# Kernel optimization log

Hardware: AMD Instinct MI355X
Metric: run time of the kernel (lower is better)

Reference implementation:

```python
import jax, jax.numpy as jnp
import numpy as np

NUM_GROUPS = 16   # static upper bound on group ids (actual ids in [0, 12))
MIN_COUNT = 10    # min_subgroup_count


def setup_inputs() -> dict:
    key = jax.random.key(0)
    ks = jax.random.split(key, 7)
    B = 32768
    N = 16777216  # dataset_size
    probs = jax.random.uniform(ks[0], (B,), dtype=jnp.float32)
    labels = jax.random.randint(ks[1], (B,), 0, 2, dtype=jnp.int32)
    groups = jax.random.randint(ks[2], (B,), 0, 12, dtype=jnp.int32)
    indices = jax.random.randint(ks[3], (B,), 0, N, dtype=jnp.int32)
    # persistent buffers, pre-filled with valid mid-epoch state
    score_buffer = jax.random.uniform(ks[4], (N,), dtype=jnp.float32)
    label_buffer = jax.random.randint(ks[5], (N,), 0, 2, dtype=jnp.int32)
    group_buffer = jax.random.randint(ks[6], (N,), 0, 12, dtype=jnp.int32)
    return {"probs": probs, "labels": labels, "groups": groups, "indices": indices,
            "score_buffer": score_buffer, "label_buffer": label_buffer,
            "group_buffer": group_buffer}


def reference(probs, labels, groups, indices, score_buffer, label_buffer, group_buffer):
    # scatter current batch into dataset-sized buffers (functional clone + write)
    scores = score_buffer.at[indices].set(probs)
    labs = label_buffer.at[indices].set(labels)
    grps = group_buffer.at[indices].set(groups)

    valid = (~jnp.isnan(scores)) & (labs >= 0) & (grps >= 0)
    scores = jnp.where(valid, scores, 0.0)        # kill NaNs before weighted sums
    seg = jnp.where(valid, grps, 0)               # invalid rows get weight 0 anyway

    def group_var(lab_val):
        # per-group mean of scores restricted to (valid & label==lab_val),
        # then unbiased variance across groups meeting the min-count threshold
        w = (valid & (labs == lab_val)).astype(scores.dtype)
        sums = jax.ops.segment_sum(scores * w, seg, num_segments=NUM_GROUPS)
        cnts = jax.ops.segment_sum(w, seg, num_segments=NUM_GROUPS)
        avg = sums / jnp.maximum(cnts, 1.0)
        incl = (cnts >= MIN_COUNT).astype(scores.dtype)
        n = incl.sum()
        mean = (avg * incl).sum() / jnp.maximum(n, 1.0)
        var = (incl * (avg - mean) ** 2).sum() / jnp.maximum(n - 1.0, 1.0)  # ddof=1
        return var, n

    pos_var, n_pos = group_var(1)
    neg_var, n_neg = group_var(0)
    pos_ok = n_pos >= 2.0
    neg_ok = n_neg >= 2.0
    loss = jnp.where(pos_ok & neg_ok, 0.5 * (pos_var + neg_var),
                     jnp.where(pos_ok, pos_var,
                               jnp.where(neg_ok, neg_var, 0.0)))
    return loss
```

## Files before the change

### kernel.cpp

```cpp
#include <hip/hip_runtime.h>
#include <hip/hip_bf16.h>


#define TBL   65536u
#define TBLM  (TBL - 1u)
#define NGR   12
#define NBK   24
#define NCOL  25
#define CCOL  26
#define NTHR  256
#define CHUNK 16384
#define ITER  (CHUNK / 4 / NTHR)
#define UNR   4
#define MINC  10.0

__device__ __forceinline__ unsigned hash_idx(unsigned idx) {
    return (idx * 2654435761u) & TBLM;
}

__global__ void k_vote(const int* __restrict__ indices,
                       unsigned long long* __restrict__ table,
                       unsigned* __restrict__ bitmap, int B) {
    int b = blockIdx.x * blockDim.x + threadIdx.x;
    if (b >= B) return;
    unsigned idx = (unsigned)indices[b];
    atomicOr(&bitmap[idx >> 5], 1u << (idx & 31u));
    unsigned long long key = ((unsigned long long)(idx + 1u)) << 32;
    unsigned long long val = key | (unsigned long long)(unsigned)b;
    unsigned slot = hash_idx(idx);
    for (;;) {
        unsigned long long prev = atomicCAS(&table[slot], 0ULL, val);
        if (prev == 0ULL) return;
        if ((prev >> 32) == (unsigned long long)(idx + 1u)) {
            atomicMax(&table[slot], val);
            return;
        }
        slot = (slot + 1u) & TBLM;
    }
}

__global__ void k_resolve(const unsigned long long* __restrict__ table,
                          const float* __restrict__ probs,
                          const int* __restrict__ labels,
                          const int* __restrict__ groups,
                          float4* __restrict__ tbl2) {
    int s = blockIdx.x * blockDim.x + threadIdx.x;
    unsigned long long e = table[s];
    unsigned hi = (unsigned)(e >> 32);
    float4 r = make_float4(0.f, 0.f, 0.f, 0.f);
    if (hi) {
        int b = (int)(e & 0xffffffffu);
        r.x = probs[b];
        r.y = __int_as_float(labels[b]);
        r.z = __int_as_float(groups[b]);
        r.w = __uint_as_float(hi);
    }
    tbl2[s] = r;
}

__device__ __forceinline__ void apply_ovr(int idx, float& s, int& l, int& g,
        const float4* __restrict__ tbl2) {
    unsigned slot = hash_idx((unsigned)idx);
    unsigned hi = (unsigned)idx + 1u;
    for (;;) {
        float4 r = tbl2[slot];
        if (__float_as_uint(r.w) == hi) {
            s = r.x; l = __float_as_int(r.y); g = __float_as_int(r.z);
            return;
        }
        slot = (slot + 1u) & TBLM;
    }
}

__device__ __forceinline__ float ovr_s(int idx,
        const float4* __restrict__ tbl2) {
    unsigned slot = hash_idx((unsigned)idx);
    unsigned hi = (unsigned)idx + 1u;
    for (;;) {
        float4 r = tbl2[slot];
        if (__float_as_uint(r.w) == hi) return r.x;
        slot = (slot + 1u) & TBLM;
    }
}

__device__ __forceinline__ void quad_p1(float* __restrict__ row,
        unsigned* __restrict__ bstr32,
        float4 s4, int4 l4, int4 g4, unsigned bits, int v,
        const float4* __restrict__ tbl2) {
    float ss[4] = {s4.x, s4.y, s4.z, s4.w};
    int   ll[4] = {l4.x, l4.y, l4.z, l4.w};
    int   gg[4] = {g4.x, g4.y, g4.z, g4.w};
    if (bits & 0xFu) {
#pragma unroll
        for (int e = 0; e < 4; ++e)
            if ((bits >> e) & 1u)
                apply_ovr((v << 2) + e, ss[e], ll[e], gg[e], tbl2);
    }
    float val[4]; int bkt[4];
#pragma unroll
    for (int e = 0; e < 4; ++e) {
        bool valid = (ss[e] == ss[e]) && ((unsigned)ll[e] < 2u) &&
                     ((unsigned)gg[e] < (unsigned)NGR);
        bkt[e] = valid ? (gg[e] * 2 + ll[e]) : NBK;
        val[e] = valid ? ss[e] : 0.f;
    }
    bstr32[v] = (unsigned)bkt[0] | ((unsigned)bkt[1] << 8) |
                ((unsigned)bkt[2] << 16) | ((unsigned)bkt[3] << 24);
#define MRG(i, j) { bool m_ = (bkt[i] == bkt[j]); \
                    val[i] += m_ ? val[j] : 0.f;  \
                    bkt[j] = m_ ? NBK : bkt[j];   \
                    val[j] = m_ ? 0.f : val[j]; }
    MRG(0,1) MRG(0,2) MRG(0,3) MRG(1,2) MRG(1,3) MRG(2,3)
#undef MRG
    float a0 = row[bkt[0]], a1 = row[bkt[1]], a2 = row[bkt[2]], a3 = row[bkt[3]];
    row[bkt[0]] = a0 + val[0];
    row[bkt[1]] = a1 + val[1];
    row[bkt[2]] = a2 + val[2];
    row[bkt[3]] = a3 + val[3];
}

__global__ __launch_bounds__(NTHR, 4) void k_pass1(
        const float* __restrict__ sb, const int* __restrict__ lb,
        const int* __restrict__ gb, const unsigned* __restrict__ bitmap,
        const float4* __restrict__ tbl2,
        float* __restrict__ bsum, unsigned char* __restrict__ bstream,
        int n, int nblk) {
    __shared__ float s_acc[NTHR * NCOL];
    int tid = threadIdx.x, blk = blockIdx.x;
    for (int i = tid; i < NTHR * NCOL; i += NTHR) s_acc[i] = 0.f;
    __syncthreads();
    float* row = &s_acc[tid * NCOL];
    unsigned* bstr32 = (unsigned*)bstream;
    int vbase = (blk * CHUNK) >> 2, nv = n >> 2;
    if (vbase + (CHUNK >> 2) <= nv) {
        int v0 = vbase + tid;
        unsigned sh = (unsigned)((v0 & 7) * 4);
#pragma unroll
        for (int m = 0; m < ITER / UNR; ++m) {
            float4 s4[UNR]; int4 l4[UNR], g4[UNR]; unsigned bm[UNR];
#pragma unroll
            for (int u = 0; u < UNR; ++u) {
                int v = v0 + (m * UNR + u) * NTHR;
                s4[u] = ((const float4*)sb)[v];
                l4[u] = ((const int4*)lb)[v];
                g4[u] = ((const int4*)gb)[v];
                bm[u] = bitmap[v >> 3];
            }
            asm volatile("" ::: "memory");
#pragma unroll
            for (int u = 0; u < UNR; ++u) {
                int v = v0 + (m * UNR + u) * NTHR;
                quad_p1(row, bstr32, s4[u], l4[u], g4[u], bm[u] >> sh, v, tbl2);
            }
        }
    } else {
        for (int it = 0; it < ITER; ++it) {
            int v = vbase + it * NTHR + tid;
            if (v >= nv) break;
            float4 s4 = ((const float4*)sb)[v];
            int4   l4 = ((const int4*)lb)[v];
            int4   g4 = ((const int4*)gb)[v];
            unsigned bits = bitmap[v >> 3] >> ((v & 7) * 4);
            quad_p1(row, bstr32, s4, l4, g4, bits, v, tbl2);
        }
    }
    if (blk == nblk - 1) {
        for (int i = (nv << 2) + tid; i < n; i += NTHR) {
            float s = sb[i]; int l = lb[i], g = gb[i];
            if ((bitmap[i >> 5] >> (i & 31)) & 1u)
                apply_ovr(i, s, l, g, tbl2);
            bool valid = (s == s) && ((unsigned)l < 2u) && ((unsigned)g < (unsigned)NGR);
            int bk = valid ? (g * 2 + l) : NBK;
            bstream[i] = (unsigned char)bk;
            row[bk] += valid ? s : 0.f;
        }
    }
    __syncthreads();
    if (tid < NBK * 8) {
        int bkt = tid >> 3, sub = tid & 7;
        float sm = 0.f;
        for (int j = 0; j < 32; ++j) sm += s_acc[(sub * 32 + j) * NCOL + bkt];
        for (int d = 4; d >= 1; d >>= 1) sm += __shfl_down(sm, d, 8);
        if (!sub) bsum[bkt * nblk + blk] = sm;
    }
}

__global__ void k_scan(const float* __restrict__ bsum,
                       float* __restrict__ bpref, int nblk) {
    __shared__ double sc[NTHR];
    int t = threadIdx.x, k = blockIdx.x;
    const float* src = bsum  + (size_t)k * nblk;
    float*       dst = bpref + (size_t)k * nblk;
    double carry = 0.0;
    for (int s0 = 0; s0 < nblk; s0 += 4 * NTHR) {
        int i0 = s0 + 4 * t;
        float x0 = (i0 + 0 < nblk) ? src[i0 + 0] : 0.f;
        float x1 = (i0 + 1 < nblk) ? src[i0 + 1] : 0.f;
        float x2 = (i0 + 2 < nblk) ? src[i0 + 2] : 0.f;
        float x3 = (i0 + 3 < nblk) ? src[i0 + 3] : 0.f;
        double p0 = (double)x0, p1 = p0 + x1, p2 = p1 + x2, tot = p2 + x3;
        sc[t] = tot;
        __syncthreads();
        for (int st = 1; st < NTHR; st <<= 1) {
            double a = (t >= st) ? sc[t - st] : 0.0;
            __syncthreads();
            sc[t] += a;
            __syncthreads();
        }
        double excl = carry + sc[t] - tot;
        if (i0 + 0 < nblk) dst[i0 + 0] = (float)excl;
        if (i0 + 1 < nblk) dst[i0 + 1] = (float)(excl + p0);
        if (i0 + 2 < nblk) dst[i0 + 2] = (float)(excl + p1);
        if (i0 + 3 < nblk) dst[i0 + 3] = (float)(excl + p2);
        double bt = sc[NTHR - 1];
        __syncthreads();
        carry += bt;
    }
}

__device__ __forceinline__ double aload_d(const double* p) {
    unsigned long long u = __hip_atomic_load((const unsigned long long*)p,
                              __ATOMIC_RELAXED, __HIP_MEMORY_SCOPE_AGENT);
    return __longlong_as_double((long long)u);
}

__device__ __forceinline__ void quad_p2(float* __restrict__ row,
        unsigned short* __restrict__ crow,
        const float2* __restrict__ s_model,
        float4 s4, unsigned b4, unsigned obits, int v, int base,
        const float4* __restrict__ tbl2) {
    float ss[4] = {s4.x, s4.y, s4.z, s4.w};
    if (obits & 0xFu) {
#pragma unroll
        for (int e = 0; e < 4; ++e)
            if ((obits >> e) & 1u) ss[e] = ovr_s((v << 2) + e, tbl2);
    }
    float cv[4]; int bkt[4], cn[4];
#pragma unroll
    for (int e = 0; e < 4; ++e) {
        int idx = (v << 2) + e;
        int bk = (int)((b4 >> (8 * e)) & 0xFFu);
        float s = ss[e];
        float2 m = s_model[bk];
        float S = fmaf(m.y, (float)(idx - base), m.x);
        float T = S + s;
        unsigned ue = __float_as_uint(T) & 0x7f800000u;
        float c;
        if (ue < (24u << 23)) c = s;
        else {
            unsigned ub = ue - (23u << 23);
            float u    = __uint_as_float(ub);
            float uinv = __uint_as_float((254u << 23) - ub);
            c = u * rintf(s * uinv);
        }
        bool valid = bk < NBK;
        bkt[e] = bk;
        cv[e] = valid ? c : 0.f;
        cn[e] = valid ? 1 : 0;
    }
#define MRG(i, j) { bool m_ = (bkt[i] == bkt[j]); \
                    cv[i] += m_ ? cv[j] : 0.f;    \
                    cn[i] += m_ ? cn[j] : 0;      \
                    bkt[j] = m_ ? NBK : bkt[j];   \
                    cv[j] = m_ ? 0.f : cv[j];     \
                    cn[j] = m_ ? 0 : cn[j]; }
    MRG(0,1) MRG(0,2) MRG(0,3) MRG(1,2) MRG(1,3) MRG(2,3)
#undef MRG
    float a0 = row[bkt[0]], a1 = row[bkt[1]], a2 = row[bkt[2]], a3 = row[bkt[3]];
    row[bkt[0]] = a0 + cv[0];
    row[bkt[1]] = a1 + cv[1];
    row[bkt[2]] = a2 + cv[2];
    row[bkt[3]] = a3 + cv[3];
    unsigned short c0 = crow[bkt[0]], c1 = crow[bkt[1]],
                   c2 = crow[bkt[2]], c3 = crow[bkt[3]];
    crow[bkt[0]] = (unsigned short)(c0 + cn[0]);
    crow[bkt[1]] = (unsigned short)(c1 + cn[1]);
    crow[bkt[2]] = (unsigned short)(c2 + cn[2]);
    crow[bkt[3]] = (unsigned short)(c3 + cn[3]);
}

__global__ __launch_bounds__(NTHR, 4) void k_pass2(
        const float* __restrict__ sb,
        const unsigned char* __restrict__ bstream,
        const unsigned* __restrict__ bitmap,
        const float4* __restrict__ tbl2,
        const float* __restrict__ bsum, const float* __restrict__ bpref,
        double* __restrict__ acc_sum, double* __restrict__ acc_cnt,
        unsigned* __restrict__ done, float* __restrict__ out,
        int n, int nblk) {
    __shared__ float s_accv[NTHR * NCOL];
    __shared__ unsigned short s_cnt[NTHR * CCOL];
    __shared__ float2 s_model[NCOL];
    int tid = threadIdx.x, blk = blockIdx.x;
    for (int i = tid; i < NTHR * NCOL; i += NTHR) s_accv[i] = 0.f;
    for (int i = tid; i < NTHR * CCOL; i += NTHR) s_cnt[i] = 0;
    if (tid < NBK)
        s_model[tid] = make_float2(bpref[tid * nblk + blk],
                                   bsum[tid * nblk + blk] * (1.0f / CHUNK));
    if (tid == NBK) s_model[NBK] = make_float2(0.f, 0.f);
    __syncthreads();
    float* row = &s_accv[tid * NCOL];
    unsigned short* crow = &s_cnt[tid * CCOL];
    const unsigned* bstr32 = (const unsigned*)bstream;
    int base = blk * CHUNK;
    int vbase = base >> 2, nv = n >> 2;
    if (vbase + (CHUNK >> 2) <= nv) {
        int v0 = vbase + tid;
        unsigned sh = (unsigned)((v0 & 7) * 4);
#pragma unroll
        for (int m = 0; m < ITER / UNR; ++m) {
            float4 s4[UNR]; unsigned pk[UNR], bm[UNR];
#pragma unroll
            for (int u = 0; u < UNR; ++u) {
                int v = v0 + (m * UNR + u) * NTHR;
                s4[u] = ((const float4*)sb)[v];
                pk[u] = bstr32[v];
                bm[u] = bitmap[v >> 3];
            }
            asm volatile("" ::: "memory");
#pragma unroll
            for (int u = 0; u < UNR; ++u) {
                int v = v0 + (m * UNR + u) * NTHR;
                quad_p2(row, crow, s_model, s4[u], pk[u], bm[u] >> sh,
                        v, base, tbl2);
            }
        }
    } else {
        for (int it = 0; it < ITER; ++it) {
            int v = vbase + it * NTHR + tid;
            if (v >= nv) break;
            float4 s4 = ((const float4*)sb)[v];
            unsigned b4 = bstr32[v];
            unsigned bits = bitmap[v >> 3] >> ((v & 7) * 4);
            quad_p2(row, crow, s_model, s4, b4, bits, v, base, tbl2);
        }
    }
    if (blk == nblk - 1) {
        for (int i = (nv << 2) + tid; i < n; i += NTHR) {
            float s = sb[i];
            int bk = (int)bstream[i];
            if ((bitmap[i >> 5] >> (i & 31)) & 1u)
                s = ovr_s(i, tbl2);
            float2 m = s_model[bk];
            float S = fmaf(m.y, (float)(i - base), m.x);
            float T = S + s;
            unsigned ue = __float_as_uint(T) & 0x7f800000u;
            float c;
            if (ue < (24u << 23)) c = s;
            else {
                unsigned ub = ue - (23u << 23);
                float u    = __uint_as_float(ub);
                float uinv = __uint_as_float((254u << 23) - ub);
                c = u * rintf(s * uinv);
            }
            bool valid = bk < NBK;
            row[bk] += valid ? c : 0.f;
            crow[bk] = (unsigned short)(crow[bk] + (valid ? 1 : 0));
        }
    }
    __syncthreads();
    if (tid < NBK * 8) {
        int bkt = tid >> 3, sub = tid & 7;
        float sm = 0.f; unsigned cc = 0;
        for (int j = 0; j < 32; ++j) {
            int t2 = sub * 32 + j;
            sm += s_accv[t2 * NCOL + bkt];
            cc += s_cnt[t2 * CCOL + bkt];
        }
        for (int d = 4; d >= 1; d >>= 1) {
            sm += __shfl_down(sm, d, 8);
            cc += __shfl_down(cc, d, 8);
        }
        if (!sub) {
            atomicAdd(&acc_sum[bkt], (double)sm);
            atomicAdd(&acc_cnt[bkt], (double)cc);
        }
    }
    __syncthreads();
    if (tid == 0) {
        __threadfence();
        unsigned r = __hip_atomic_fetch_add(done, 1u, __ATOMIC_ACQ_REL,
                                            __HIP_MEMORY_SCOPE_AGENT);
        if (r == (unsigned)(gridDim.x - 1)) {
            double var[2], nn[2];
            for (int l = 0; l < 2; ++l) {
                double avg[NGR];
                double ncnt = 0.0, s = 0.0;
                for (int g = 0; g < NGR; ++g) {
                    double c  = aload_d(&acc_cnt[g * 2 + l]);
                    double sm = aload_d(&acc_sum[g * 2 + l]);
                    double a = sm / fmax(c, 1.0);
                    avg[g] = a;
                    if (c >= MINC) { ncnt += 1.0; s += a; }
                }
                double mean = s / fmax(ncnt, 1.0), v = 0.0;
                for (int g = 0; g < NGR; ++g) {
                    double c = aload_d(&acc_cnt[g * 2 + l]);
                    if (c >= MINC) { double d = avg[g] - mean; v += d * d; }
                }
                var[l] = v / fmax(ncnt - 1.0, 1.0);
                nn[l] = ncnt;
            }
            bool p = nn[1] >= 2.0, q = nn[0] >= 2.0;
            double loss = (p && q) ? 0.5 * (var[1] + var[0])
                        : (p ? var[1] : (q ? var[0] : 0.0));
            out[0] = (float)loss;
        }
    }
}

extern "C" void kernel_launch(void* const* d_in, const int* in_sizes, int n_in,
                              void* d_out, int out_size, void* d_ws, size_t ws_size,
                              hipStream_t stream) {
    const float* probs   = (const float*)d_in[0];
    const int*   labels  = (const int*)d_in[1];
    const int*   groups  = (const int*)d_in[2];
    const int*   indices = (const int*)d_in[3];
    const float* sb      = (const float*)d_in[4];
    const int*   lb      = (const int*)d_in[5];
    const int*   gb      = (const int*)d_in[6];
    int B = in_sizes[0];
    int n = in_sizes[4];
    int nblk   = (n + CHUNK - 1) / CHUNK;
    int nwords = (n + 31) / 32;

    char* ws = (char*)d_ws;
    size_t off = 0;
    unsigned long long* table = (unsigned long long*)(ws + off); off += (size_t)TBL * 8;
    unsigned* bitmap  = (unsigned*)(ws + off); off += (size_t)nwords * 4;
    off = (off + 15) & ~(size_t)15;
    double*   acc_sum = (double*)(ws + off);   off += NBK * 8;
    double*   acc_cnt = (double*)(ws + off);   off += NBK * 8;
    unsigned* done    = (unsigned*)(ws + off); off += 16;
    size_t zero_bytes = off;
    float4*   tbl2    = (float4*)(ws + off);   off += (size_t)TBL * 16;
    unsigned char* bstream = (unsigned char*)(ws + off);
    off += ((size_t)n + 15) & ~(size_t)15;
    float*    bsum    = (float*)(ws + off);    off += (size_t)nblk * NBK * 4;
    float*    bpref   = (float*)(ws + off);    off += (size_t)nblk * NBK * 4;

    hipMemsetAsync(d_ws, 0, zero_bytes, stream);

    dim3 bblk((B + NTHR - 1) / NTHR);
    hipLaunchKernelGGL(k_vote, bblk, dim3(NTHR), 0, stream,
                       indices, table, bitmap, B);
    hipLaunchKernelGGL(k_resolve, dim3(TBL / NTHR), dim3(NTHR), 0, stream,
                       table, probs, labels, groups, tbl2);
    hipLaunchKernelGGL(k_pass1, dim3(nblk), dim3(NTHR), 0, stream,
                       sb, lb, gb, bitmap, tbl2, bsum, bstream, n, nblk);
    hipLaunchKernelGGL(k_scan, dim3(NBK), dim3(NTHR), 0, stream,
                       bsum, bpref, nblk);
    hipLaunchKernelGGL(k_pass2, dim3(nblk), dim3(NTHR), 0, stream,
                       sb, bstream, bitmap, tbl2, bsum, bpref,
                       acc_sum, acc_cnt, done, (float*)d_out, n, nblk);
}
```

Baseline: 305.1 us.

## Move overridden-row handling out of the streaming loops into a sparse bitmap sweep

Overridden rows are now marked invalid (bucket NBK) in the pass-1 stream, and both passes process them afterwards in a separate per-block sweep. That sweep walks bitmap words with ctz and does the hash lookups there. This removes per-quad bitmap loads and divergent hash probing from the hot loops of pass 2, and lets pass 2 unroll deeper (8 instead of 4). The cost is an extra bitmap scan per block. The quantisation term for overridden rows is still computed against the block prefix model, but its in-chunk order differs from the original, which could change rounding slightly.

```diff
diff --git a/kernel.cpp b/kernel.cpp
--- a/kernel.cpp
+++ b/kernel.cpp
@@ -11,7 +11,8 @@
 #define NTHR  256
 #define CHUNK 16384
 #define ITER  (CHUNK / 4 / NTHR)
-#define UNR   4
+#define UNR1  4
+#define UNR2  8
 #define MINC  10.0
 
 __device__ __forceinline__ unsigned hash_idx(unsigned idx) {
@@ -72,34 +73,17 @@
     }
 }
 
-__device__ __forceinline__ float ovr_s(int idx,
-        const float4* __restrict__ tbl2) {
-    unsigned slot = hash_idx((unsigned)idx);
-    unsigned hi = (unsigned)idx + 1u;
-    for (;;) {
-        float4 r = tbl2[slot];
-        if (__float_as_uint(r.w) == hi) return r.x;
-        slot = (slot + 1u) & TBLM;
-    }
-}
-
 __device__ __forceinline__ void quad_p1(float* __restrict__ row,
         unsigned* __restrict__ bstr32,
-        float4 s4, int4 l4, int4 g4, unsigned bits, int v,
-        const float4* __restrict__ tbl2) {
+        float4 s4, int4 l4, int4 g4, unsigned bits, int v) {
     float ss[4] = {s4.x, s4.y, s4.z, s4.w};
     int   ll[4] = {l4.x, l4.y, l4.z, l4.w};
     int   gg[4] = {g4.x, g4.y, g4.z, g4.w};
-    if (bits & 0xFu) {
-#pragma unroll
-        for (int e = 0; e < 4; ++e)
-            if ((bits >> e) & 1u)
-                apply_ovr((v << 2) + e, ss[e], ll[e], gg[e], tbl2);
-    }
     float val[4]; int bkt[4];
 #pragma unroll
     for (int e = 0; e < 4; ++e) {
-        bool valid = (ss[e] == ss[e]) && ((unsigned)ll[e] < 2u) &&
+        bool ov = (bits >> e) & 1u;
+        bool valid = !ov && (ss[e] == ss[e]) && ((unsigned)ll[e] < 2u) &&
                      ((unsigned)gg[e] < (unsigned)NGR);
         bkt[e] = valid ? (gg[e] * 2 + ll[e]) : NBK;
         val[e] = valid ? ss[e] : 0.f;
@@ -136,11 +120,11 @@
         int v0 = vbase + tid;
         unsigned sh = (unsigned)((v0 & 7) * 4);
 #pragma unroll
-        for (int m = 0; m < ITER / UNR; ++m) {
-            float4 s4[UNR]; int4 l4[UNR], g4[UNR]; unsigned bm[UNR];
-#pragma unroll
-            for (int u = 0; u < UNR; ++u) {
-                int v = v0 + (m * UNR + u) * NTHR;
+        for (int m = 0; m < ITER / UNR1; ++m) {
+            float4 s4[UNR1]; int4 l4[UNR1], g4[UNR1]; unsigned bm[UNR1];
+#pragma unroll
+            for (int u = 0; u < UNR1; ++u) {
+                int v = v0 + (m * UNR1 + u) * NTHR;
                 s4[u] = ((const float4*)sb)[v];
                 l4[u] = ((const int4*)lb)[v];
                 g4[u] = ((const int4*)gb)[v];
@@ -148,9 +132,9 @@
             }
             asm volatile("" ::: "memory");
 #pragma unroll
-            for (int u = 0; u < UNR; ++u) {
-                int v = v0 + (m * UNR + u) * NTHR;
-                quad_p1(row, bstr32, s4[u], l4[u], g4[u], bm[u] >> sh, v, tbl2);
+            for (int u = 0; u < UNR1; ++u) {
+                int v = v0 + (m * UNR1 + u) * NTHR;
+                quad_p1(row, bstr32, s4[u], l4[u], g4[u], bm[u] >> sh, v);
             }
         }
     } else {
@@ -161,7 +145,7 @@
             int4   l4 = ((const int4*)lb)[v];
             int4   g4 = ((const int4*)gb)[v];
             unsigned bits = bitmap[v >> 3] >> ((v & 7) * 4);
-            quad_p1(row, bstr32, s4, l4, g4, bits, v, tbl2);
+            quad_p1(row, bstr32, s4, l4, g4, bits, v);
         }
     }
     if (blk == nblk - 1) {
@@ -173,6 +157,25 @@
             int bk = valid ? (g * 2 + l) : NBK;
             bstream[i] = (unsigned char)bk;
             row[bk] += valid ? s : 0.f;
+        }
+    }
+    {
+        int wbase = (blk * CHUNK) >> 5;
+        int hotend = nv << 2;
+        for (int w = wbase + tid; w < wbase + CHUNK / 32; w += NTHR) {
+            unsigned bits = ((w << 5) < n) ? bitmap[w] : 0u;
+            while (bits) {
+                int b = __builtin_ctz(bits);
+                bits &= bits - 1u;
+                int idx = (w << 5) + b;
+                if (idx >= hotend) continue;
+                float s; int l, g;
+                apply_ovr(idx, s, l, g, tbl2);
+                bool valid = (s == s) && ((unsigned)l < 2u) &&
+                             ((unsigned)g < (unsigned)NGR);
+                int bk = valid ? (g * 2 + l) : NBK;
+                row[bk] += valid ? s : 0.f;
+            }
         }
     }
     __syncthreads();
@@ -224,35 +227,28 @@
     return __longlong_as_double((long long)u);
 }
 
+__device__ __forceinline__ float quantc(float s, float2 m, int off) {
+    float S = fmaf(m.y, (float)off, m.x);
+    float T = S + s;
+    unsigned ue = __float_as_uint(T) & 0x7f800000u;
+    unsigned ub = ue - (23u << 23);
+    float u    = __uint_as_float(ub);
+    float uinv = __uint_as_float((254u << 23) - ub);
+    float cq   = u * rintf(s * uinv);
+    return (ue < (24u << 23)) ? s : cq;
+}
+
 __device__ __forceinline__ void quad_p2(float* __restrict__ row,
         unsigned short* __restrict__ crow,
         const float2* __restrict__ s_model,
-        float4 s4, unsigned b4, unsigned obits, int v, int base,
-        const float4* __restrict__ tbl2) {
+        float4 s4, unsigned b4, int v, int base) {
     float ss[4] = {s4.x, s4.y, s4.z, s4.w};
-    if (obits & 0xFu) {
-#pragma unroll
-        for (int e = 0; e < 4; ++e)
-            if ((obits >> e) & 1u) ss[e] = ovr_s((v << 2) + e, tbl2);
-    }
     float cv[4]; int bkt[4], cn[4];
 #pragma unroll
     for (int e = 0; e < 4; ++e) {
         int idx = (v << 2) + e;
         int bk = (int)((b4 >> (8 * e)) & 0xFFu);
-        float s = ss[e];
-        float2 m = s_model[bk];
-        float S = fmaf(m.y, (float)(idx - base), m.x);
-        float T = S + s;
-        unsigned ue = __float_as_uint(T) & 0x7f800000u;
-        float c;
-        if (ue < (24u << 23)) c = s;
-        else {
-            unsigned ub = ue - (23u << 23);
-            float u    = __uint_as_float(ub);
-            float uinv = __uint_as_float((254u << 23) - ub);
-            c = u * rintf(s * uinv);
-        }
+        float c = quantc(ss[e], s_model[bk], idx - base);
         bool valid = bk < NBK;
         bkt[e] = bk;
         cv[e] = valid ? c : 0.f;
@@ -293,7 +289,10 @@
     __shared__ float2 s_model[NCOL];
     int tid = threadIdx.x, blk = blockIdx.x;
     for (int i = tid; i < NTHR * NCOL; i += NTHR) s_accv[i] = 0.f;
-    for (int i = tid; i < NTHR * CCOL; i += NTHR) s_cnt[i] = 0;
+    {
+        unsigned* cz = (unsigned*)s_cnt;
+        for (int i = tid; i < NTHR * CCOL / 2; i += NTHR) cz[i] = 0u;
+    }
     if (tid < NBK)
         s_model[tid] = make_float2(bpref[tid * nblk + blk],
                                    bsum[tid * nblk + blk] * (1.0f / CHUNK));
@@ -306,23 +305,20 @@
     int vbase = base >> 2, nv = n >> 2;
     if (vbase + (CHUNK >> 2) <= nv) {
         int v0 = vbase + tid;
-        unsigned sh = (unsigned)((v0 & 7) * 4);
-#pragma unroll
-        for (int m = 0; m < ITER / UNR; ++m) {
-            float4 s4[UNR]; unsigned pk[UNR], bm[UNR];
-#pragma unroll
-            for (int u = 0; u < UNR; ++u) {
-                int v = v0 + (m * UNR + u) * NTHR;
+#pragma unroll
+        for (int m = 0; m < ITER / UNR2; ++m) {
+            float4 s4[UNR2]; unsigned pk[UNR2];
+#pragma unroll
+            for (int u = 0; u < UNR2; ++u) {
+                int v = v0 + (m * UNR2 + u) * NTHR;
                 s4[u] = ((const float4*)sb)[v];
                 pk[u] = bstr32[v];
-                bm[u] = bitmap[v >> 3];
             }
             asm volatile("" ::: "memory");
 #pragma unroll
-            for (int u = 0; u < UNR; ++u) {
-                int v = v0 + (m * UNR + u) * NTHR;
-                quad_p2(row, crow, s_model, s4[u], pk[u], bm[u] >> sh,
-                        v, base, tbl2);
+            for (int u = 0; u < UNR2; ++u) {
+                int v = v0 + (m * UNR2 + u) * NTHR;
+                quad_p2(row, crow, s_model, s4[u], pk[u], v, base);
             }
         }
     } else {
@@ -331,31 +327,45 @@
             if (v >= nv) break;
             float4 s4 = ((const float4*)sb)[v];
             unsigned b4 = bstr32[v];
-            unsigned bits = bitmap[v >> 3] >> ((v & 7) * 4);
-            quad_p2(row, crow, s_model, s4, b4, bits, v, base, tbl2);
+            quad_p2(row, crow, s_model, s4, b4, v, base);
         }
     }
     if (blk == nblk - 1) {
         for (int i = (nv << 2) + tid; i < n; i += NTHR) {
             float s = sb[i];
             int bk = (int)bstream[i];
-            if ((bitmap[i >> 5] >> (i & 31)) & 1u)
-                s = ovr_s(i, tbl2);
-            float2 m = s_model[bk];
-            float S = fmaf(m.y, (float)(i - base), m.x);
-            float T = S + s;
-            unsigned ue = __float_as_uint(T) & 0x7f800000u;
-            float c;
-            if (ue < (24u << 23)) c = s;
-            else {
-                unsigned ub = ue - (23u << 23);
-                float u    = __uint_as_float(ub);
-                float uinv = __uint_as_float((254u << 23) - ub);
-                c = u * rintf(s * uinv);
-            }
+            if ((bitmap[i >> 5] >> (i & 31)) & 1u) {
+                int l, g;
+                apply_ovr(i, s, l, g, tbl2);
+                bool va = (s == s) && ((unsigned)l < 2u) &&
+                          ((unsigned)g < (unsigned)NGR);
+                bk = va ? (g * 2 + l) : NBK;
+            }
+            float c = quantc(s, s_model[bk], i - base);
             bool valid = bk < NBK;
             row[bk] += valid ? c : 0.f;
             crow[bk] = (unsigned short)(crow[bk] + (valid ? 1 : 0));
+        }
+    }
+    {
+        int wbase = (blk * CHUNK) >> 5;
+        int hotend = nv << 2;
+        for (int w = wbase + tid; w < wbase + CHUNK / 32; w += NTHR) {
+            unsigned bits = ((w << 5) < n) ? bitmap[w] : 0u;
+            while (bits) {
+                int b = __builtin_ctz(bits);
+                bits &= bits - 1u;
+                int idx = (w << 5) + b;
+                if (idx >= hotend) continue;
+                float s; int l, g;
+                apply_ovr(idx, s, l, g, tbl2);
+                bool valid = (s == s) && ((unsigned)l < 2u) &&
+                             ((unsigned)g < (unsigned)NGR);
+                int bk = valid ? (g * 2 + l) : NBK;
+                float c = quantc(s, s_model[bk], idx - base);
+                row[bk] += valid ? c : 0.f;
+                crow[bk] = (unsigned short)(crow[bk] + (valid ? 1 : 0));
+            }
         }
     }
     __syncthreads();
```

New measurement: 303.7 us. No clear change (-0.5%).
